# Kernel tuning notes

Measured on AMD Instinct MI355X. Metric: run time of the kernel, lower is better.

The kernel has to match this reference:

```python
import jax, jax.numpy as jnp
import numpy as np
from jax import lax

B, T, I = 64, 128, 128   # batch, encoder time, signal features
H = 512                  # lstm hidden size
V = 32                   # vocab = len(output_dict); SOS=0, EOS=1
L = 64                   # decode steps = target_onehot.shape[1]


def lstm_cell(x, h, c, Wih, Whh, bih, bhh):
    # PyTorch gate order: i, f, g, o. x:[B,in], h/c:[B,H]
    g = x @ Wih.T + h @ Whh.T + (bih + bhh)
    i, f, gg, o = jnp.split(g, 4, axis=-1)
    c_new = jax.nn.sigmoid(f) * c + jax.nn.sigmoid(i) * jnp.tanh(gg)
    h_new = jax.nn.sigmoid(o) * jnp.tanh(c_new)
    return h_new, c_new


def setup_inputs() -> dict:
    key = jax.random.key(0)
    ks = jax.random.split(key, 16)
    s = 1.0 / np.sqrt(H)
    u = lambda k, shape: jax.random.uniform(k, shape, jnp.float32, -s, s)
    inp = {}
    inp["signal"] = jax.random.normal(ks[0], (B, T, I), jnp.float32)
    tgt_ids = jax.random.randint(ks[1], (B, L), 0, V)
    inp["target_onehot"] = jax.nn.one_hot(tgt_ids, V, dtype=jnp.float32)
    # encoder bi-LSTM params, stacked [2(dir), ...]
    inp["enc_Wih"] = u(ks[2], (2, 4 * H, I))
    inp["enc_Whh"] = u(ks[3], (2, 4 * H, H))
    inp["enc_bih"] = u(ks[4], (2, 4 * H))
    inp["enc_bhh"] = u(ks[5], (2, 4 * H))
    # decoder bi-LSTM params
    inp["dec_Wih"] = u(ks[6], (2, 4 * H, V))
    inp["dec_Whh"] = u(ks[7], (2, 4 * H, H))
    inp["dec_bih"] = u(ks[8], (2, 4 * H))
    inp["dec_bhh"] = u(ks[9], (2, 4 * H))
    # output projection Linear(2H -> V)
    so = 1.0 / np.sqrt(2 * H)
    inp["W_out"] = jax.random.uniform(ks[10], (V, 2 * H), jnp.float32, -so, so)
    inp["b_out"] = jax.random.uniform(ks[11], (V,), jnp.float32, -so, so)
    return inp


def _forward(signal, target_onehot, enc_Wih, enc_Whh, enc_bih, enc_bhh,
             dec_Wih, dec_Whh, dec_bih, dec_bhh, W_out, b_out):
    Bv = signal.shape[0]
    zeros = jnp.zeros((Bv, H), signal.dtype)
    xs = jnp.swapaxes(signal, 0, 1)  # [T,B,I]

    def enc_step(d):
        def f(carry, x):
            h, c = carry
            h, c = lstm_cell(x, h, c, enc_Wih[d], enc_Whh[d], enc_bih[d], enc_bhh[d])
            return (h, c), None
        return f

    # forward direction final state; backward direction runs on reversed seq
    (hf, cf), _ = lax.scan(enc_step(0), (zeros, zeros), xs)
    (hb, cb), _ = lax.scan(enc_step(1), (zeros, zeros), xs[::-1])

    def dec_step(carry, _):
        inp, hf, cf, hb, cb = carry
        x = jax.nn.relu(inp)  # relu of one-hot (identity, kept for fidelity)
        hf, cf = lstm_cell(x, hf, cf, dec_Wih[0], dec_Whh[0], dec_bih[0], dec_bhh[0])
        hb, cb = lstm_cell(x, hb, cb, dec_Wih[1], dec_Whh[1], dec_bih[1], dec_bhh[1])
        logits = jnp.concatenate([hf, hb], axis=-1) @ W_out.T + b_out  # [B,V]
        # teacher forcing prob is 0 in the source -> always greedy one-hot feedback
        nxt = jax.nn.one_hot(jnp.argmax(logits, axis=-1), V, dtype=logits.dtype)
        return (nxt, hf, cf, hb, cb), logits

    init = (target_onehot[:, 0], hf, cf, hb, cb)
    _, logits = lax.scan(dec_step, init, None, length=target_onehot.shape[1])
    logits = jnp.swapaxes(logits, 0, 1)  # [B,L,V]
    return jax.nn.log_softmax(logits, axis=-1)


def reference(signal, target_onehot, enc_Wih, enc_Whh, enc_bih, enc_bhh,
              dec_Wih, dec_Whh, dec_bih, dec_bhh, W_out, b_out):
    return _forward(signal, target_onehot, enc_Wih, enc_Whh, enc_bih, enc_bhh,
                    dec_Wih, dec_Whh, dec_bih, dec_bhh, W_out, b_out)
```

## Files before the change

kernel.cpp:

```cpp
#include <hip/hip_runtime.h>
#include <math.h>

#define DEV __device__ __forceinline__
typedef __attribute__((ext_vector_type(4))) float f32x4;

constexpr int BATCH = 64;
constexpr int TSTEP = 128;
constexpr int IDIM  = 128;
constexpr int HDIM  = 512;
constexpr int VDIM  = 32;
constexpr int LDEC  = 64;
constexpr int NBLK  = 256;
constexpr int BDIM  = 256;
constexpr unsigned MAGIC = 0x1357BD1u;
constexpr unsigned SPIN_LIMIT = 1u << 22;

constexpr size_t OFF_BAR  = 0;
constexpr size_t OFF_SIGT = 1024;
constexpr size_t OFF_HT   = OFF_SIGT + (size_t)TSTEP*IDIM*BATCH*4;
constexpr size_t OFF_XD   = OFF_HT   + (size_t)2*2*HDIM*BATCH*4;
constexpr size_t WS_NEED  = OFF_XD   + (size_t)VDIM*BATCH*4;

DEV float ald(const float* p){ return __hip_atomic_load(p, __ATOMIC_RELAXED, __HIP_MEMORY_SCOPE_AGENT); }
DEV void  ast(float* p, float v){ __hip_atomic_store(p, v, __ATOMIC_RELAXED, __HIP_MEMORY_SCOPE_AGENT); }
DEV void  wait_vm0(){ asm volatile("s_waitcnt vmcnt(0)" ::: "memory"); }
DEV f32x4 gl4_sc1(const float* p){ f32x4 r; asm volatile("global_load_dwordx4 %0, %1, off sc1" : "=v"(r) : "v"(p)); return r; }
DEV f32x4 gl4_pln(const float* p){ f32x4 r; asm volatile("global_load_dwordx4 %0, %1, off"     : "=v"(r) : "v"(p)); return r; }
DEV float gl1_sc1(const float* p){ float r; asm volatile("global_load_dword %0, %1, off sc1"   : "=v"(r) : "v"(p)); return r; }

DEV void gbar_full(unsigned* cnt, unsigned* gen, unsigned nb, unsigned* dead) {
  __syncthreads();
  if (threadIdx.x == 0) {
    unsigned g = __hip_atomic_load(gen, __ATOMIC_RELAXED, __HIP_MEMORY_SCOPE_AGENT);
    unsigned a = __hip_atomic_fetch_add(cnt, 1u, __ATOMIC_ACQ_REL, __HIP_MEMORY_SCOPE_AGENT);
    if (a >= nb - 1u) {
      __hip_atomic_store(cnt, 0u, __ATOMIC_RELAXED, __HIP_MEMORY_SCOPE_AGENT);
      __hip_atomic_fetch_add(gen, 1u, __ATOMIC_RELEASE, __HIP_MEMORY_SCOPE_AGENT);
    } else {
      unsigned spins = 0;
      while (__hip_atomic_load(gen, __ATOMIC_RELAXED, __HIP_MEMORY_SCOPE_AGENT) == g) {
        __builtin_amdgcn_s_sleep(1);
        if ((++spins & 255u) == 0u) {
          if (__hip_atomic_load(dead, __ATOMIC_RELAXED, __HIP_MEMORY_SCOPE_AGENT) != 0u) break;
          if (spins > SPIN_LIMIT) { __hip_atomic_store(dead, 1u, __ATOMIC_RELAXED, __HIP_MEMORY_SCOPE_AGENT); break; }
        }
      }
      (void)__hip_atomic_load(gen, __ATOMIC_ACQUIRE, __HIP_MEMORY_SCOPE_AGENT);
    }
  }
  __syncthreads();
}

DEV void fastbar(unsigned* cnt, unsigned* gen, unsigned nb, unsigned* dead) {
  wait_vm0();
  __syncthreads();
  if (threadIdx.x == 0) {
    unsigned g = __hip_atomic_load(gen, __ATOMIC_RELAXED, __HIP_MEMORY_SCOPE_AGENT);
    unsigned a = __hip_atomic_fetch_add(cnt, 1u, __ATOMIC_RELAXED, __HIP_MEMORY_SCOPE_AGENT);
    if (a >= nb - 1u) {
      __hip_atomic_store(cnt, 0u, __ATOMIC_RELAXED, __HIP_MEMORY_SCOPE_AGENT);
      __hip_atomic_fetch_add(gen, 1u, __ATOMIC_RELAXED, __HIP_MEMORY_SCOPE_AGENT);
    } else {
      unsigned spins = 0;
      while (__hip_atomic_load(gen, __ATOMIC_RELAXED, __HIP_MEMORY_SCOPE_AGENT) == g) {
        __builtin_amdgcn_s_sleep(1);
        if ((++spins & 255u) == 0u) {
          if (__hip_atomic_load(dead, __ATOMIC_RELAXED, __HIP_MEMORY_SCOPE_AGENT) != 0u) break;
          if (spins > SPIN_LIMIT) { __hip_atomic_store(dead, 1u, __ATOMIC_RELAXED, __HIP_MEMORY_SCOPE_AGENT); break; }
        }
      }
    }
  }
  __syncthreads();
}

template<int KX, bool XSC1>
DEV void cell_step(float acc[4], const float* __restrict__ xsrc,
                   const float* __restrict__ hcur,
                   const float* const* wx, const float* const* wh,
                   int b, int tid, float* __restrict__ buf)
{
  constexpr int  NXC = KX / 64;
  constexpr bool XR  = (KX % 64) != 0;
  constexpr int  NC  = NXC + (XR ? 1 : 0) + HDIM / 64;
  f32x4 r[4];

  auto issue = [&](int c) {
    if (c < NXC) {
      const float* s = xsrc + (size_t)c*4096 + tid*4;
      #pragma unroll
      for (int q = 0; q < 4; ++q) r[q] = XSC1 ? gl4_sc1(s + q*1024) : gl4_pln(s + q*1024);
    } else if (XR && c == NXC) {
      const float* s = xsrc + tid*4;
      #pragma unroll
      for (int q = 0; q < 2; ++q) r[q] = XSC1 ? gl4_sc1(s + q*1024) : gl4_pln(s + q*1024);
    } else {
      const int ch = c - NXC - (XR ? 1 : 0);
      const float* s = hcur + (size_t)ch*4096 + tid*4;
      #pragma unroll
      for (int q = 0; q < 4; ++q) r[q] = gl4_sc1(s + q*1024);
    }
  };

  issue(0);
  for (int c = 0; c < NC; ++c) {
    wait_vm0();
    float* dst = buf + (c & 1)*4096;
    const bool small = (XR && c == NXC);
    *(f32x4*)(dst + tid*4)        = r[0];
    *(f32x4*)(dst + tid*4 + 1024) = r[1];
    if (!small) {
      *(f32x4*)(dst + tid*4 + 2048) = r[2];
      *(f32x4*)(dst + tid*4 + 3072) = r[3];
    }
    __syncthreads();
    if (c + 1 < NC) issue(c + 1);
    const float *g0, *g1, *g2, *g3;
    if (c < NXC)            { g0=wx[0]+c*64; g1=wx[1]+c*64; g2=wx[2]+c*64; g3=wx[3]+c*64; }
    else if (XR && c==NXC)  { g0=wx[0];      g1=wx[1];      g2=wx[2];      g3=wx[3]; }
    else { const int ch=c-NXC-(XR?1:0); g0=wh[0]+ch*64; g1=wh[1]+ch*64; g2=wh[2]+ch*64; g3=wh[3]+ch*64; }
    const float* bs = dst + b;
    if (!small) {
      #pragma unroll
      for (int kk = 0; kk < 64; ++kk) {
        float xv = bs[kk*64];
        acc[0] += g0[kk]*xv; acc[1] += g1[kk]*xv; acc[2] += g2[kk]*xv; acc[3] += g3[kk]*xv;
      }
    } else {
      #pragma unroll
      for (int kk = 0; kk < 32; ++kk) {
        float xv = bs[kk*64];
        acc[0] += g0[kk]*xv; acc[1] += g1[kk]*xv; acc[2] += g2[kk]*xv; acc[3] += g3[kk]*xv;
      }
    }
  }
}

__global__ void __launch_bounds__(BDIM)
encdec(const float* __restrict__ signal, const float* __restrict__ tgt,
       const float* __restrict__ eWih, const float* __restrict__ eWhh,
       const float* __restrict__ eBih, const float* __restrict__ eBhh,
       const float* __restrict__ dWih, const float* __restrict__ dWhh,
       const float* __restrict__ dBih, const float* __restrict__ dBhh,
       const float* __restrict__ Wout, const float* __restrict__ bOut,
       float* __restrict__ out,
       unsigned* __restrict__ bar, float* __restrict__ sigT,
       float* __restrict__ hT, float* __restrict__ xdT)
{
  __shared__ __align__(16) float buf[2*4096];
  __shared__ float red[BDIM];
  const int blk = blockIdx.x, tid = threadIdx.x;
  const int d  = blk >> 7;
  const int js = blk & 127;
  const int b  = tid & 63;
  const int jj = tid >> 6;
  const int j  = js * 4 + jj;

  unsigned* dead = bar + 224;
  if (blk == 0 && tid == 0) {
    #pragma unroll
    for (int q = 1; q <= 7; ++q)
      __hip_atomic_store(bar + q*32, 0u, __ATOMIC_RELAXED, __HIP_MEMORY_SCOPE_AGENT);
    __hip_atomic_store(bar, MAGIC, __ATOMIC_RELEASE, __HIP_MEMORY_SCOPE_AGENT);
  }
  if (tid == 0) {
    unsigned spins = 0;
    while (__hip_atomic_load(bar, __ATOMIC_RELAXED, __HIP_MEMORY_SCOPE_AGENT) != MAGIC) {
      __builtin_amdgcn_s_sleep(1);
      if (++spins > SPIN_LIMIT) break;
    }
    (void)__hip_atomic_load(bar, __ATOMIC_ACQUIRE, __HIP_MEMORY_SCOPE_AGENT);
  }
  __syncthreads();
  unsigned *jc = bar + 32, *jg = bar + 64;
  unsigned *dc = bar + (d ? 160 : 96), *dg = bar + (d ? 192 : 128);

  {
    const int t = blk & 127, ih = blk >> 7;
    float* tile = buf;
    for (int idx = tid; idx < 64*64; idx += BDIM) {
      int il = idx & 63, bb = idx >> 6;
      tile[il*65 + bb] = signal[((size_t)bb*TSTEP + t)*IDIM + ih*64 + il];
    }
    __syncthreads();
    for (int idx = tid; idx < 64*64; idx += BDIM) {
      int bb = idx & 63, il = idx >> 6;
      sigT[((size_t)t*IDIM + ih*64 + il)*64 + bb] = tile[il*65 + bb];
    }
  }
  ast(&hT[((size_t)(0*2 + d)*HDIM + j)*64 + b], 0.f);
  ast(&hT[((size_t)(1*2 + d)*HDIM + j)*64 + b], 0.f);
  if (blk < BATCH && tid < VDIM) {
    float tv = tgt[((size_t)blk*LDEC)*VDIM + tid];
    ast(&xdT[tid*64 + blk], tv > 0.f ? tv : 0.f);
  }
  gbar_full(jc, jg, NBLK, dead);

  const float* wx[4]; const float* wh[4]; float bsum[4];
  #pragma unroll
  for (int g = 0; g < 4; ++g) {
    int r = __builtin_amdgcn_readfirstlane(g*HDIM + j);
    wx[g] = eWih + ((size_t)d*4*HDIM + r)*IDIM;
    wh[g] = eWhh + ((size_t)d*4*HDIM + r)*HDIM;
    bsum[g] = eBih[d*4*HDIM + r] + eBhh[d*4*HDIM + r];
  }
  float c = 0.f;
  for (int t = 0; t < TSTEP; ++t) {
    const int cur = t & 1, nxt = cur ^ 1;
    const int td = d ? (TSTEP - 1 - t) : t;
    float acc[4] = {0.f, 0.f, 0.f, 0.f};
    cell_step<IDIM, false>(acc, sigT + (size_t)td*IDIM*64,
                           hT + ((size_t)(cur*2 + d)*HDIM)*64, wx, wh, b, tid, buf);
    float gi = acc[0]+bsum[0], gf = acc[1]+bsum[1], gg = acc[2]+bsum[2], go = acc[3]+bsum[3];
    float si = 1.f/(1.f+expf(-gi)), sf = 1.f/(1.f+expf(-gf)), so = 1.f/(1.f+expf(-go));
    c = sf*c + si*tanhf(gg);
    ast(&hT[((size_t)(nxt*2 + d)*HDIM + j)*64 + b], so*tanhf(c));
    fastbar(dc, dg, 128u, dead);
  }
  fastbar(jc, jg, NBLK, dead);

  #pragma unroll
  for (int g = 0; g < 4; ++g) {
    int r = __builtin_amdgcn_readfirstlane(g*HDIM + j);
    wx[g] = dWih + ((size_t)d*4*HDIM + r)*VDIM;
    wh[g] = dWhh + ((size_t)d*4*HDIM + r)*HDIM;
    bsum[g] = dBih[d*4*HDIM + r] + dBhh[d*4*HDIM + r];
  }
  for (int s = 0; s < LDEC; ++s) {
    const int cur = s & 1, nxt = cur ^ 1;
    float acc[4] = {0.f, 0.f, 0.f, 0.f};
    cell_step<VDIM, true>(acc, xdT, hT + ((size_t)(cur*2 + d)*HDIM)*64, wx, wh, b, tid, buf);
    float gi = acc[0]+bsum[0], gf = acc[1]+bsum[1], gg = acc[2]+bsum[2], go = acc[3]+bsum[3];
    float si = 1.f/(1.f+expf(-gi)), sf = 1.f/(1.f+expf(-gf)), so = 1.f/(1.f+expf(-go));
    c = sf*c + si*tanhf(gg);
    ast(&hT[((size_t)(nxt*2 + d)*HDIM + j)*64 + b], so*tanhf(c));
    fastbar(jc, jg, NBLK, dead);

    if (blk < BATCH) {
      const int bb = blk, v = tid & 31, kc = tid >> 5;
      const float* hx = hT + (size_t)nxt*2*HDIM*64 + bb;
      float part = 0.f;
      float rr[32];
      for (int w = 0; w < 4; ++w) {
        #pragma unroll
        for (int i = 0; i < 32; ++i)
          rr[i] = gl1_sc1(hx + (size_t)(kc*128 + w*32 + i)*64);
        wait_vm0();
        #pragma unroll
        for (int i = 0; i < 32; ++i)
          part += Wout[(size_t)v*(2*HDIM) + kc*128 + w*32 + i] * rr[i];
      }
      red[tid] = part;
      __syncthreads();
      if (tid < VDIM) {
        float lg = red[tid];
        #pragma unroll
        for (int q = 1; q < 8; ++q) lg += red[tid + q*32];
        lg += bOut[tid];
        float m = lg; int mi = tid;
        #pragma unroll
        for (int off = 16; off >= 1; off >>= 1) {
          float om = __shfl_xor(m, off, 64);
          int omi  = __shfl_xor(mi, off, 64);
          if (om > m || (om == m && omi < mi)) { m = om; mi = omi; }
        }
        float ex = expf(lg - m), ssum = ex;
        #pragma unroll
        for (int off = 16; off >= 1; off >>= 1) ssum += __shfl_xor(ssum, off, 64);
        out[((size_t)bb*LDEC + s)*VDIM + tid] = lg - m - logf(ssum);
        ast(&xdT[tid*64 + bb], (tid == mi) ? 1.f : 0.f);
      }
    }
    fastbar(jc, jg, NBLK, dead);
  }
}

extern "C" void kernel_launch(void* const* d_in, const int* in_sizes, int n_in,
                              void* d_out, int out_size, void* d_ws, size_t ws_size,
                              hipStream_t stream) {
  if (ws_size < WS_NEED) return;
  char* base = (char*)d_ws;
  hipLaunchKernelGGL(encdec, dim3(NBLK), dim3(BDIM), 0, stream,
    (const float*)d_in[0],  (const float*)d_in[1],
    (const float*)d_in[2],  (const float*)d_in[3],
    (const float*)d_in[4],  (const float*)d_in[5],
    (const float*)d_in[6],  (const float*)d_in[7],
    (const float*)d_in[8],  (const float*)d_in[9],
    (const float*)d_in[10], (const float*)d_in[11],
    (float*)d_out,
    (unsigned*)(base + OFF_BAR), (float*)(base + OFF_SIGT),
    (float*)(base + OFF_HT),     (float*)(base + OFF_XD));
}
```

Baseline: 4.769 ms.

## Replace flat grid barriers with two-level hierarchical counter barriers

```diff
diff --git a/kernel.cpp b/kernel.cpp
--- a/kernel.cpp
+++ b/kernel.cpp
@@ -16,59 +16,63 @@
 constexpr unsigned SPIN_LIMIT = 1u << 22;
 
 constexpr size_t OFF_BAR  = 0;
-constexpr size_t OFF_SIGT = 1024;
+constexpr size_t OFF_SIGT = 4096;
 constexpr size_t OFF_HT   = OFF_SIGT + (size_t)TSTEP*IDIM*BATCH*4;
 constexpr size_t OFF_XD   = OFF_HT   + (size_t)2*2*HDIM*BATCH*4;
 constexpr size_t WS_NEED  = OFF_XD   + (size_t)VDIM*BATCH*4;
 
-DEV float ald(const float* p){ return __hip_atomic_load(p, __ATOMIC_RELAXED, __HIP_MEMORY_SCOPE_AGENT); }
-DEV void  ast(float* p, float v){ __hip_atomic_store(p, v, __ATOMIC_RELAXED, __HIP_MEMORY_SCOPE_AGENT); }
-DEV void  wait_vm0(){ asm volatile("s_waitcnt vmcnt(0)" ::: "memory"); }
+
+DEV unsigned ldu(const unsigned* p){ return __hip_atomic_load(p, __ATOMIC_RELAXED, __HIP_MEMORY_SCOPE_AGENT); }
+DEV void     stu(unsigned* p, unsigned v){ __hip_atomic_store(p, v, __ATOMIC_RELAXED, __HIP_MEMORY_SCOPE_AGENT); }
+DEV unsigned fau(unsigned* p, unsigned v){ return __hip_atomic_fetch_add(p, v, __ATOMIC_RELAXED, __HIP_MEMORY_SCOPE_AGENT); }
+DEV void     ast(float* p, float v){ __hip_atomic_store(p, v, __ATOMIC_RELAXED, __HIP_MEMORY_SCOPE_AGENT); }
+DEV void wait_vm0(){ asm volatile("s_waitcnt vmcnt(0)" ::: "memory"); }
 DEV f32x4 gl4_sc1(const float* p){ f32x4 r; asm volatile("global_load_dwordx4 %0, %1, off sc1" : "=v"(r) : "v"(p)); return r; }
 DEV f32x4 gl4_pln(const float* p){ f32x4 r; asm volatile("global_load_dwordx4 %0, %1, off"     : "=v"(r) : "v"(p)); return r; }
 DEV float gl1_sc1(const float* p){ float r; asm volatile("global_load_dword %0, %1, off sc1"   : "=v"(r) : "v"(p)); return r; }
 
+DEV void spin_ge(const unsigned* p, unsigned tgt, unsigned* dead) {
+  unsigned spins = 0;
+  while (ldu(p) < tgt) {
+    __builtin_amdgcn_s_sleep(1);
+    if ((++spins & 255u) == 0u) {
+      if (ldu(dead)) break;
+      if (spins > SPIN_LIMIT) { stu(dead, 1u); break; }
+    }
+  }
+}
+
+DEV void hbar(unsigned* bar, int gline, int grp, int ngrp, unsigned grpsz, int genline, unsigned* dead) {
+  wait_vm0();
+  __syncthreads();
+  if (threadIdx.x == 0) {
+    unsigned* gen = bar + genline*32;
+    unsigned g = ldu(gen);
+    unsigned* gc = bar + (gline + grp)*32;
+    unsigned a = fau(gc, 1u);
+    bool rel = false;
+    if (a == grpsz - 1u) {
+      stu(gc, 0u);
+      unsigned* rt = bar + (gline + ngrp)*32;
+      unsigned ra = fau(rt, 1u);
+      if (ra == (unsigned)ngrp - 1u) { stu(rt, 0u); fau(gen, 1u); rel = true; }
+    }
+    if (!rel) spin_ge(gen, g + 1u, dead);
+  }
+  __syncthreads();
+}
+
 DEV void gbar_full(unsigned* cnt, unsigned* gen, unsigned nb, unsigned* dead) {
   __syncthreads();
   if (threadIdx.x == 0) {
-    unsigned g = __hip_atomic_load(gen, __ATOMIC_RELAXED, __HIP_MEMORY_SCOPE_AGENT);
+    unsigned g = ldu(gen);
     unsigned a = __hip_atomic_fetch_add(cnt, 1u, __ATOMIC_ACQ_REL, __HIP_MEMORY_SCOPE_AGENT);
     if (a >= nb - 1u) {
-      __hip_atomic_store(cnt, 0u, __ATOMIC_RELAXED, __HIP_MEMORY_SCOPE_AGENT);
+      stu(cnt, 0u);
       __hip_atomic_fetch_add(gen, 1u, __ATOMIC_RELEASE, __HIP_MEMORY_SCOPE_AGENT);
     } else {
-      unsigned spins = 0;
-      while (__hip_atomic_load(gen, __ATOMIC_RELAXED, __HIP_MEMORY_SCOPE_AGENT) == g) {
-        __builtin_amdgcn_s_sleep(1);
-        if ((++spins & 255u) == 0u) {
-          if (__hip_atomic_load(dead, __ATOMIC_RELAXED, __HIP_MEMORY_SCOPE_AGENT) != 0u) break;
-          if (spins > SPIN_LIMIT) { __hip_atomic_store(dead, 1u, __ATOMIC_RELAXED, __HIP_MEMORY_SCOPE_AGENT); break; }
-        }
-      }
+      spin_ge(gen, g + 1u, dead);
       (void)__hip_atomic_load(gen, __ATOMIC_ACQUIRE, __HIP_MEMORY_SCOPE_AGENT);
-    }
-  }
-  __syncthreads();
-}
-
-DEV void fastbar(unsigned* cnt, unsigned* gen, unsigned nb, unsigned* dead) {
-  wait_vm0();
-  __syncthreads();
-  if (threadIdx.x == 0) {
-    unsigned g = __hip_atomic_load(gen, __ATOMIC_RELAXED, __HIP_MEMORY_SCOPE_AGENT);
-    unsigned a = __hip_atomic_fetch_add(cnt, 1u, __ATOMIC_RELAXED, __HIP_MEMORY_SCOPE_AGENT);
-    if (a >= nb - 1u) {
-      __hip_atomic_store(cnt, 0u, __ATOMIC_RELAXED, __HIP_MEMORY_SCOPE_AGENT);
-      __hip_atomic_fetch_add(gen, 1u, __ATOMIC_RELAXED, __HIP_MEMORY_SCOPE_AGENT);
-    } else {
-      unsigned spins = 0;
-      while (__hip_atomic_load(gen, __ATOMIC_RELAXED, __HIP_MEMORY_SCOPE_AGENT) == g) {
-        __builtin_amdgcn_s_sleep(1);
-        if ((++spins & 255u) == 0u) {
-          if (__hip_atomic_load(dead, __ATOMIC_RELAXED, __HIP_MEMORY_SCOPE_AGENT) != 0u) break;
-          if (spins > SPIN_LIMIT) { __hip_atomic_store(dead, 1u, __ATOMIC_RELAXED, __HIP_MEMORY_SCOPE_AGENT); break; }
-        }
-      }
     }
   }
   __syncthreads();
@@ -156,11 +160,9 @@
   const int jj = tid >> 6;
   const int j  = js * 4 + jj;
 
-  unsigned* dead = bar + 224;
+  unsigned* dead = bar + 11*32;
   if (blk == 0 && tid == 0) {
-    #pragma unroll
-    for (int q = 1; q <= 7; ++q)
-      __hip_atomic_store(bar + q*32, 0u, __ATOMIC_RELAXED, __HIP_MEMORY_SCOPE_AGENT);
+    for (int q = 1; q <= 30; ++q) stu(bar + q*32, 0u);
     __hip_atomic_store(bar, MAGIC, __ATOMIC_RELEASE, __HIP_MEMORY_SCOPE_AGENT);
   }
   if (tid == 0) {
@@ -172,8 +174,6 @@
     (void)__hip_atomic_load(bar, __ATOMIC_ACQUIRE, __HIP_MEMORY_SCOPE_AGENT);
   }
   __syncthreads();
-  unsigned *jc = bar + 32, *jg = bar + 64;
-  unsigned *dc = bar + (d ? 160 : 96), *dg = bar + (d ? 192 : 128);
 
   {
     const int t = blk & 127, ih = blk >> 7;
@@ -194,7 +194,7 @@
     float tv = tgt[((size_t)blk*LDEC)*VDIM + tid];
     ast(&xdT[tid*64 + blk], tv > 0.f ? tv : 0.f);
   }
-  gbar_full(jc, jg, NBLK, dead);
+  gbar_full(bar + 29*32, bar + 30*32, NBLK, dead);
 
   const float* wx[4]; const float* wh[4]; float bsum[4];
   #pragma unroll
@@ -215,9 +215,9 @@
     float si = 1.f/(1.f+expf(-gi)), sf = 1.f/(1.f+expf(-gf)), so = 1.f/(1.f+expf(-go));
     c = sf*c + si*tanhf(gg);
     ast(&hT[((size_t)(nxt*2 + d)*HDIM + j)*64 + b], so*tanhf(c));
-    fastbar(dc, dg, 128u, dead);
-  }
-  fastbar(jc, jg, NBLK, dead);
+    hbar(bar, d ? 18 : 12, (blk >> 5) & 3, 4, 32u, d ? 23 : 17, dead);
+  }
+  hbar(bar, 1, blk & 7, 8, 32u, 10, dead);
 
   #pragma unroll
   for (int g = 0; g < 4; ++g) {
@@ -234,7 +234,7 @@
     float si = 1.f/(1.f+expf(-gi)), sf = 1.f/(1.f+expf(-gf)), so = 1.f/(1.f+expf(-go));
     c = sf*c + si*tanhf(gg);
     ast(&hT[((size_t)(nxt*2 + d)*HDIM + j)*64 + b], so*tanhf(c));
-    fastbar(jc, jg, NBLK, dead);
+    hbar(bar, 1, blk & 7, 8, 32u, 10, dead);
 
     if (blk < BATCH) {
       const int bb = blk, v = tid & 31, kc = tid >> 5;
@@ -271,7 +271,7 @@
         ast(&xdT[tid*64 + bb], (tid == mi) ? 1.f : 0.f);
       }
     }
-    fastbar(jc, jg, NBLK, dead);
+    hbar(bar, 1, blk & 7, 8, 32u, 10, dead);
   }
 }
 
```

New measurement: 4.670 ms. 1.02x faster.
